# Performance work log

Measured on AMD Instinct MI355X. Metric: run time of the kernel, lower is better.

## Reference

```python
import jax, jax.numpy as jnp
import numpy as np
from jax import lax

silu = jax.nn.silu

def conv2d(x, w, b, pad):
    y = lax.conv_general_dilated(x, w, (1, 1), [(pad, pad), (pad, pad)],
                                 dimension_numbers=('NCHW', 'OIHW', 'NCHW'))
    return y + b[None, :, None, None]

def avgpool2(x):
    B, C, H, W = x.shape
    return x.reshape(B, C, H // 2, 2, W // 2, 2).mean(axis=(3, 5))

def up2x(x):
    # bilinear scale_factor=2, align_corners=True (matches F.interpolate)
    B, C, H, W = x.shape
    Ho, Wo = 2 * H, 2 * W
    ys = jnp.arange(Ho, dtype=x.dtype) * ((H - 1) / (Ho - 1))
    xs = jnp.arange(Wo, dtype=x.dtype) * ((W - 1) / (Wo - 1))
    y0 = jnp.floor(ys).astype(jnp.int32); y1 = jnp.minimum(y0 + 1, H - 1); wy = ys - y0
    x0 = jnp.floor(xs).astype(jnp.int32); x1 = jnp.minimum(x0 + 1, W - 1); wx = xs - x0
    row = x[:, :, y0, :] * (1 - wy)[None, None, :, None] + x[:, :, y1, :] * wy[None, None, :, None]
    return row[:, :, :, x0] * (1 - wx) + row[:, :, :, x1] * wx

def deform_conv2d(x, offset, weight, groups):
    # torchvision DeformConv2d semantics: stride=1, pad=(k-1)//2, dilation=1, no bias
    B, Cin, H, W = x.shape
    Cout, cpg, kh, kw = weight.shape  # cpg = Cin // groups
    K = kh * kw
    OG = offset.shape[1] // (2 * K)   # offset groups
    Cog = Cin // OG
    off = offset.reshape(B, OG, K, 2, H, W)  # (dy, dx) per kernel tap
    ki = jnp.repeat(jnp.arange(kh, dtype=x.dtype) - (kh - 1) // 2, kw)  # [K]
    kj = jnp.tile(jnp.arange(kw, dtype=x.dtype) - (kw - 1) // 2, kh)
    py = off[:, :, :, 0] + jnp.arange(H, dtype=x.dtype)[None, None, None, :, None] + ki[None, None, :, None, None]
    px = off[:, :, :, 1] + jnp.arange(W, dtype=x.dtype)[None, None, None, None, :] + kj[None, None, :, None, None]
    y0f = jnp.floor(py); x0f = jnp.floor(px)
    ly = py - y0f; lx = px - x0f
    y0 = y0f.astype(jnp.int32); x0 = x0f.astype(jnp.int32)
    xg = x.reshape(B, OG, Cog, H * W)

    def corner(yi, xi, wt):
        valid = (yi >= 0) & (yi < H) & (xi >= 0) & (xi < W)
        idx = jnp.clip(yi, 0, H - 1) * W + jnp.clip(xi, 0, W - 1)        # [B,OG,K,H,W]
        idxf = jnp.broadcast_to(idx.reshape(B, OG, 1, K * H * W), (B, OG, Cog, K * H * W))
        v = jnp.take_along_axis(xg, idxf, axis=3).reshape(B, OG, Cog, K, H, W)
        return v * (wt * valid)[:, :, None]

    val = (corner(y0, x0, (1 - ly) * (1 - lx)) + corner(y0, x0 + 1, (1 - ly) * lx)
           + corner(y0 + 1, x0, ly * (1 - lx)) + corner(y0 + 1, x0 + 1, ly * lx))
    # grouped contraction over sampled taps
    valg = val.reshape(B, groups, Cin // groups, K, H, W)
    wg = weight.reshape(groups, Cout // groups, cpg, K)
    return jnp.einsum('bgckhw,gock->bgohw', valg, wg).reshape(B, Cout, H, W)

def setup_inputs() -> dict:
    key = jax.random.key(0)
    ks = iter(jax.random.split(key, 64))
    def w(shape, s=0.05):
        return jax.random.normal(next(ks), shape, jnp.float32) * s
    B, H, W = 4, 512, 512
    d = {'x': jax.random.normal(next(ks), (B, 4, H, W), jnp.float32)}
    # offset estimators (small scale so sampled offsets stay moderate)
    d['eo1_w1'] = w((18, 4, 5, 5), 0.02);  d['eo1_b1'] = w((18,), 0.02)
    d['eo1_w2'] = w((36, 18, 5, 5), 0.02); d['eo1_b2'] = w((36,), 0.02)
    d['dcw1'] = w((2, 2, 3, 3))            # DeformConv2d(4->2, groups=2)
    d['c1d_w1'] = w((4, 2, 3, 3));   d['c1d_b1'] = w((4,))
    d['c1d_w2'] = w((8, 4, 3, 3));   d['c1d_b2'] = w((8,))
    d['eo2_w1'] = w((18, 8, 5, 5), 0.02);  d['eo2_b1'] = w((18,), 0.02)
    d['eo2_w2'] = w((36, 18, 5, 5), 0.02); d['eo2_b2'] = w((36,), 0.02)
    d['dcw2'] = w((8, 4, 3, 3))            # DeformConv2d(8->8, groups=2)
    d['c2d_w1'] = w((12, 8, 3, 3));  d['c2d_b1'] = w((12,))
    d['c2d_w2'] = w((16, 12, 3, 3)); d['c2d_b2'] = w((16,))
    d['eo3_w1'] = w((18, 16, 5, 5), 0.02); d['eo3_b1'] = w((18,), 0.02)
    d['eo3_w2'] = w((36, 18, 5, 5), 0.02); d['eo3_b2'] = w((36,), 0.02)
    d['dcw3'] = w((16, 8, 3, 3))           # DeformConv2d(16->16, groups=2)
    d['c3d_w1'] = w((14, 16, 3, 3)); d['c3d_b1'] = w((14,))
    d['c3d_w2'] = w((12, 14, 3, 3)); d['c3d_b2'] = w((12,))
    d['up2_w'] = w((12, 12, 3, 3));  d['up2_b'] = w((12,))
    d['c2u_w1'] = w((16, 28, 3, 3)); d['c2u_b1'] = w((16,))
    d['c2u_w2'] = w((8, 16, 3, 3));  d['c2u_b2'] = w((8,))
    d['up1_w'] = w((8, 8, 3, 3));    d['up1_b'] = w((8,))
    d['c1u_w1'] = w((8, 16, 3, 3));  d['c1u_b1'] = w((8,))
    d['c1u_w2'] = w((2, 8, 3, 3));   d['c1u_b2'] = w((2,))
    return d

def reference(x, eo1_w1, eo1_b1, eo1_w2, eo1_b2, dcw1, c1d_w1, c1d_b1, c1d_w2, c1d_b2,
              eo2_w1, eo2_b1, eo2_w2, eo2_b2, dcw2, c2d_w1, c2d_b1, c2d_w2, c2d_b2,
              eo3_w1, eo3_b1, eo3_w2, eo3_b2, dcw3, c3d_w1, c3d_b1, c3d_w2, c3d_b2,
              up2_w, up2_b, c2u_w1, c2u_b1, c2u_w2, c2u_b2, up1_w, up1_b,
              c1u_w1, c1u_b1, c1u_w2, c1u_b2):
    def convbasic(h, w1, b1, w2, b2):
        return silu(conv2d(silu(conv2d(h, w1, b1, 1)), w2, b2, 1))
    # level 1 down
    off1 = conv2d(conv2d(x, eo1_w1, eo1_b1, 2), eo1_w2, eo1_b2, 2)
    comp1 = deform_conv2d(x, off1, dcw1, groups=2)
    conv1_d = convbasic(comp1, c1d_w1, c1d_b1, c1d_w2, c1d_b2)
    pool1 = avgpool2(conv1_d)
    # level 2 down
    off2 = conv2d(conv2d(pool1, eo2_w1, eo2_b1, 2), eo2_w2, eo2_b2, 2)
    comp2 = deform_conv2d(pool1, off2, dcw2, groups=2)
    conv2_d = convbasic(comp2, c2d_w1, c2d_b1, c2d_w2, c2d_b2)
    pool2 = avgpool2(conv2_d)
    # level 3 (bottleneck)
    off3 = conv2d(conv2d(pool2, eo3_w1, eo3_b1, 2), eo3_w2, eo3_b2, 2)
    comp3 = deform_conv2d(pool2, off3, dcw3, groups=2)
    conv3_d = convbasic(comp3, c3d_w1, c3d_b1, c3d_w2, c3d_b2)
    # up path
    usmpl2 = silu(conv2d(up2x(conv3_d), up2_w, up2_b, 1))
    conv2_u = convbasic(jnp.concatenate([usmpl2, conv2_d], axis=1), c2u_w1, c2u_b1, c2u_w2, c2u_b2)
    usmpl1 = silu(conv2d(up2x(conv2_u), up1_w, up1_b, 1))
    conv1_u = convbasic(jnp.concatenate([usmpl1, conv1_d], axis=1), c1u_w1, c1u_b1, c1u_w2, c1u_b2)
    return conv1_u
```

## Files before the change

kernel.cpp:

```cpp
#include <hip/hip_runtime.h>
#include <math.h>

#define THREADS 256
typedef __attribute__((ext_vector_type(2))) float f32x2;
typedef __attribute__((ext_vector_type(4))) float f32x4;

__device__ __forceinline__ float silu_f(float v) {
    return v / (1.f + __expf(-v));
}

__device__ __forceinline__ void pk_fma_lo(f32x2& d, f32x2 a, f32x2 b) {
    asm("v_pk_fma_f32 %0, %1, %2, %0 op_sel:[0,0,0] op_sel_hi:[0,1,1]"
        : "+v"(d) : "v"(a), "v"(b));
}
__device__ __forceinline__ void pk_fma_hi(f32x2& d, f32x2 a, f32x2 b) {
    asm("v_pk_fma_f32 %0, %1, %2, %0 op_sel:[1,0,0] op_sel_hi:[1,1,1]"
        : "+v"(d) : "v"(a), "v"(b));
}

struct TEnt { const float* src; int dst; int cin; int cout; int k2; int base; int n; };
struct TTab { TEnt e[40]; int total; };

__global__ __launch_bounds__(THREADS)
void transpose_w_k(TTab t, float* __restrict__ tw) {
    const int i = blockIdx.x * THREADS + threadIdx.x;
    if (i >= t.total) return;
    int j = 0;
    while (i >= t.e[j].base + t.e[j].n) ++j;
    const TEnt e = t.e[j];
    const int local = i - e.base;
    const int co  = local % e.cout;
    const int tmp = local / e.cout;
    const int k   = tmp % e.k2;
    const int ci  = tmp / e.k2;
    tw[e.dst + local] = e.src[(co * e.cin + ci) * e.k2 + k];
}

template<int KS, int PX>
__device__ __forceinline__ void load_row(float* __restrict__ rr,
                                         const float* __restrict__ rp,
                                         bool vy, int x0, int W)
{
    constexpr int PAD = (KS - 1) / 2;
    constexpr int RW = PX + KS - 1;
#pragma unroll
    for (int q = -1; q <= PX / 4; ++q) {
        if (4 * q + 3 + PAD < 0 || 4 * q + PAD >= RW) continue;
        const int xs = x0 + 4 * q;
        float vc[4] = {0.f, 0.f, 0.f, 0.f};
        if (vy && xs >= 0 && xs + 4 <= W) {
            const float4 v = *reinterpret_cast<const float4*>(rp + xs);
            vc[0] = v.x; vc[1] = v.y; vc[2] = v.z; vc[3] = v.w;
        } else if (vy) {
#pragma unroll
            for (int c = 0; c < 4; ++c)
                vc[c] = ((unsigned)(xs + c) < (unsigned)W) ? rp[xs + c] : 0.f;
        }
#pragma unroll
        for (int c = 0; c < 4; ++c) {
            const int t = 4 * q + c + PAD;
            if (t >= 0 && t < RW) rr[t] = vc[c];
        }
    }
}

template<int CIN, int COUT, int KS, int PX, int PHASE, int RW2, int WQ, int NP>
__device__ __forceinline__ void chan_body(
    const float* __restrict__ ip0, const float* __restrict__ sw,
    int cl, int y, int x0, int W, int H, int lw, int total,
    f32x2 (&r2)[2][RW2], f32x4 (&wb)[2][WQ], f32x2 (&acc)[NP][PX])
{
    constexpr int PAD = (KS - 1) / 2;
    constexpr int K2 = KS * KS;
    constexpr int CO_S = (COUT + 3) & ~3;
#pragma unroll
    for (int ky = 0; ky < KS; ++ky) {
        {
            const bool last = (ky + 1 == KS);
            const int ncl = cl + (last ? 1 : 0);
            const int nky = last ? 0 : (ky + 1);
            if (!last || ncl < CIN) {
                const int yy = y + nky - PAD;
                load_row<KS, PX>((float*)r2[(PHASE + ky + 1) & 1],
                                 ip0 + (size_t)ncl * total + (yy << lw),
                                 (unsigned)yy < (unsigned)H, x0, W);
            }
        }
#pragma unroll
        for (int kx = 0; kx < KS; ++kx) {
            const int t = ky * KS + kx;
            const int wc = (PHASE + t) & 1;
            if (t + 1 < K2 || cl + 1 < CIN) {
                const f32x4* __restrict__ nx =
                    (const f32x4*)(sw + (size_t)(cl * K2 + t + 1) * CO_S);
#pragma unroll
                for (int q = 0; q < WQ; ++q) wb[wc ^ 1][q] = nx[q];
            }
#pragma unroll
            for (int q = 0; q < WQ; ++q) {
                const f32x4 w4 = wb[wc][q];
                const f32x2 wlo = __builtin_shufflevector(w4, w4, 0, 1);
                const f32x2 whi = __builtin_shufflevector(w4, w4, 2, 3);
#pragma unroll
                for (int s = 0; s < 2; ++s) {
                    const int p = 2 * q + s;
                    if (p < NP) {
                        const f32x2 wp = s ? whi : wlo;
#pragma unroll
                        for (int j = 0; j < PX; ++j) {
                            const int e = kx + j;
                            if (e & 1) pk_fma_hi(acc[p][j], r2[(PHASE + ky) & 1][e >> 1], wp);
                            else       pk_fma_lo(acc[p][j], r2[(PHASE + ky) & 1][e >> 1], wp);
                        }
                    }
                }
            }
            __builtin_amdgcn_sched_barrier(0);
        }
    }
}

template<int CIN, int COUT, int KS, bool ACT, int PX>
__global__ __launch_bounds__(THREADS)
void conv_sl_k(const float* __restrict__ in, const float* __restrict__ wt,
               const float* __restrict__ bias, float* __restrict__ out,
               int H, int lw, int bs_in, int bs_out, int nb, int nz)
{
    constexpr int PAD = (KS - 1) / 2;
    constexpr int K2 = KS * KS;
    constexpr int CO_S = (COUT + 3) & ~3;
    constexpr int WQ = CO_S / 4;
    constexpr int NP = COUT / 2;
    constexpr int RW = PX + KS - 1;
    constexpr int RW2 = (RW + 1) / 2;
    static_assert(CIN % 2 == 0 && COUT % 2 == 0 && PX % 4 == 0, "");
    __shared__ float sw[CIN * K2 * CO_S];

    int lin = blockIdx.x;
    const int z = lin % nz; lin /= nz;
    const int b = lin % nb; lin /= nb;
    const int xb = lin;

    const float* __restrict__ wz = wt + (size_t)z * (CIN * K2 * COUT);
    const int W = 1 << lw;
    const int total = H << lw;
    const int idx = (xb * THREADS + threadIdx.x) * PX;
    const float* ip0 = in + (size_t)b * bs_in;
    float* op = out + (size_t)b * bs_out + (size_t)z * COUT * total;
    const int x0 = idx & (W - 1);
    const int y  = idx >> lw;

    for (int i = threadIdx.x; i < CIN * K2 * COUT; i += THREADS)
        sw[(i / COUT) * CO_S + i % COUT] = wz[i];
    __syncthreads();

    f32x2 acc[NP][PX];
#pragma unroll
    for (int p = 0; p < NP; ++p) {
        f32x2 bb;
        bb.x = bias[z * COUT + 2 * p];
        bb.y = bias[z * COUT + 2 * p + 1];
#pragma unroll
        for (int j = 0; j < PX; ++j) acc[p][j] = bb;
    }

    f32x2 r2[2][RW2];
    f32x4 wb[2][WQ];
    {
        const int yy = y - PAD;
        load_row<KS, PX>((float*)r2[0], ip0 + (yy << lw),
                         (unsigned)yy < (unsigned)H, x0, W);
        const f32x4* __restrict__ w0 = (const f32x4*)sw;
#pragma unroll
        for (int q = 0; q < WQ; ++q) wb[0][q] = w0[q];
    }

#pragma unroll 1
    for (int c2 = 0; c2 < CIN / 2; ++c2) {
        chan_body<CIN, COUT, KS, PX, 0, RW2, WQ, NP>(ip0, sw, 2 * c2,     y, x0, W, H, lw, total, r2, wb, acc);
        chan_body<CIN, COUT, KS, PX, 1, RW2, WQ, NP>(ip0, sw, 2 * c2 + 1, y, x0, W, H, lw, total, r2, wb, acc);
    }

#pragma unroll
    for (int p = 0; p < NP; ++p) {
#pragma unroll
        for (int h = 0; h < 2; ++h) {
            const int co = 2 * p + h;
#pragma unroll
            for (int j4 = 0; j4 < PX / 4; ++j4) {
                float4 v;
                float a0 = h ? acc[p][4 * j4 + 0].y : acc[p][4 * j4 + 0].x;
                float a1 = h ? acc[p][4 * j4 + 1].y : acc[p][4 * j4 + 1].x;
                float a2 = h ? acc[p][4 * j4 + 2].y : acc[p][4 * j4 + 2].x;
                float a3 = h ? acc[p][4 * j4 + 3].y : acc[p][4 * j4 + 3].x;
                v.x = ACT ? silu_f(a0) : a0;
                v.y = ACT ? silu_f(a1) : a1;
                v.z = ACT ? silu_f(a2) : a2;
                v.w = ACT ? silu_f(a3) : a3;
                *reinterpret_cast<float4*>(op + (size_t)co * total + idx + 4 * j4) = v;
            }
        }
    }
}

template<int CIN, int COUT, int KS, bool ACT, int PX>
__global__ __launch_bounds__(THREADS)
void conv_k(const float* __restrict__ in, const float* __restrict__ wt,
            const float* __restrict__ bias, float* __restrict__ out,
            int H, int lw, int bs_in, int bs_out)
{
    constexpr int PAD = (KS - 1) / 2;
    constexpr int K2 = KS * KS;
    constexpr int CO_S = (COUT + 3) & ~3;
    constexpr int WQ = CO_S / 4;
    constexpr int NP = COUT / 2;
    constexpr int RW = PX + KS - 1;
    constexpr int RW2 = (RW + 1) / 2;
    static_assert(COUT % 2 == 0, "");
    __shared__ float sw[CIN * K2 * CO_S];

    const int W = 1 << lw;
    const int total = H << lw;
    const int idx = (blockIdx.x * THREADS + threadIdx.x) * PX;
    const float* ip0 = in + (size_t)blockIdx.y * bs_in;
    float* op = out + (size_t)blockIdx.y * bs_out;
    const int x0 = idx & (W - 1);
    const int y  = idx >> lw;

    for (int i = threadIdx.x; i < CIN * K2 * COUT; i += THREADS)
        sw[(i / COUT) * CO_S + i % COUT] = wt[i];
    __syncthreads();

    f32x2 acc[NP][PX];
#pragma unroll
    for (int p = 0; p < NP; ++p) {
        f32x2 bb;
        bb.x = bias[2 * p];
        bb.y = bias[2 * p + 1];
#pragma unroll
        for (int j = 0; j < PX; ++j) acc[p][j] = bb;
    }

#pragma unroll 1
    for (int cl = 0; cl < CIN; ++cl) {
        const float* __restrict__ row0 = ip0 + (size_t)cl * total;
        f32x2 r2[KS][RW2];
#pragma unroll
        for (int ky = 0; ky < KS; ++ky) {
            const int yy = y + ky - PAD;
            load_row<KS, PX>((float*)r2[ky], row0 + (yy << lw),
                             (unsigned)yy < (unsigned)H, x0, W);
        }
        const float* __restrict__ wbase = &sw[cl * K2 * CO_S];
#pragma unroll
        for (int t = 0; t < K2; ++t) {
            const int ky = t / KS, kx = t % KS;
            const f32x4* __restrict__ wv = (const f32x4*)(wbase + t * CO_S);
#pragma unroll
            for (int q = 0; q < WQ; ++q) {
                const f32x4 w4 = wv[q];
                const f32x2 wlo = __builtin_shufflevector(w4, w4, 0, 1);
                const f32x2 whi = __builtin_shufflevector(w4, w4, 2, 3);
#pragma unroll
                for (int s = 0; s < 2; ++s) {
                    const int p = 2 * q + s;
                    if (p < NP) {
                        const f32x2 wp = s ? whi : wlo;
#pragma unroll
                        for (int j = 0; j < PX; ++j) {
                            const int e = kx + j;
                            if (e & 1) pk_fma_hi(acc[p][j], r2[ky][e >> 1], wp);
                            else       pk_fma_lo(acc[p][j], r2[ky][e >> 1], wp);
                        }
                    }
                }
            }
            __builtin_amdgcn_sched_barrier(0);
        }
    }

#pragma unroll
    for (int p = 0; p < NP; ++p) {
#pragma unroll
        for (int h = 0; h < 2; ++h) {
            const int co = 2 * p + h;
            if (PX == 2) {
                float2 v;
                float a0 = h ? acc[p][0].y : acc[p][0].x;
                float a1 = h ? acc[p][1].y : acc[p][1].x;
                v.x = ACT ? silu_f(a0) : a0;
                v.y = ACT ? silu_f(a1) : a1;
                *reinterpret_cast<float2*>(op + (size_t)co * total + idx) = v;
            } else {
#pragma unroll
                for (int j4 = 0; j4 < PX / 4; ++j4) {
                    float4 v;
                    float a0 = h ? acc[p][4 * j4 + 0].y : acc[p][4 * j4 + 0].x;
                    float a1 = h ? acc[p][4 * j4 + 1].y : acc[p][4 * j4 + 1].x;
                    float a2 = h ? acc[p][4 * j4 + 2].y : acc[p][4 * j4 + 2].x;
                    float a3 = h ? acc[p][4 * j4 + 3].y : acc[p][4 * j4 + 3].x;
                    v.x = ACT ? silu_f(a0) : a0;
                    v.y = ACT ? silu_f(a1) : a1;
                    v.z = ACT ? silu_f(a2) : a2;
                    v.w = ACT ? silu_f(a3) : a3;
                    *reinterpret_cast<float4*>(op + (size_t)co * total + idx + 4 * j4) = v;
                }
            }
        }
    }
}

template<int CIN, int COUT>
__global__ __launch_bounds__(THREADS)
void dconv_k(const float* __restrict__ in, const float* __restrict__ off,
             const float* __restrict__ twg0, const float* __restrict__ twg1,
             float* __restrict__ out,
             int H, int lw, int bs_in, int bs_off, int bs_out)
{
    constexpr int K = 9;
    constexpr int OG = 2;
    constexpr int COG = CIN / OG;
    constexpr int COUTG = COUT / 2;
    constexpr int NWG = COG * K * COUTG;
    __shared__ float sw[2 * NWG];
    for (int i = threadIdx.x; i < 2 * NWG; i += THREADS)
        sw[i] = (i < NWG) ? twg0[i] : twg1[i - NWG];
    __syncthreads();

    const int W = 1 << lw;
    const int total = H << lw;
    const int idx = blockIdx.x * THREADS + threadIdx.x;
    const float* ip0 = in + (size_t)blockIdx.y * bs_in;
    const float* offp = off + (size_t)blockIdx.y * bs_off;
    float* op = out + (size_t)blockIdx.y * bs_out;
    const int x = idx & (W - 1);
    const int y = idx >> lw;

    float acc[COUT];
#pragma unroll
    for (int co = 0; co < COUT; ++co) acc[co] = 0.f;

#pragma unroll
    for (int og = 0; og < OG; ++og) {
#pragma unroll
        for (int k = 0; k < K; ++k) {
            const int ki = k / 3 - 1;
            const int kj = k % 3 - 1;
            const float dy = offp[(size_t)(((og * K + k) * 2 + 0)) * total + idx];
            const float dx = offp[(size_t)(((og * K + k) * 2 + 1)) * total + idx];
            const float py = dy + (float)(y + ki);
            const float px = dx + (float)(x + kj);
            const float y0f = floorf(py), x0f = floorf(px);
            const float ly = py - y0f, lx = px - x0f;
            const int y0 = (int)y0f, x0 = (int)x0f;
            const int y1 = y0 + 1, x1 = x0 + 1;
            const bool vy0 = (unsigned)y0 < (unsigned)H;
            const bool vy1 = (unsigned)y1 < (unsigned)H;
            const bool vx0 = (unsigned)x0 < (unsigned)W;
            const bool vx1 = (unsigned)x1 < (unsigned)W;
            const int cy0 = min(max(y0, 0), H - 1), cy1 = min(max(y1, 0), H - 1);
            const int cx0 = min(max(x0, 0), W - 1), cx1 = min(max(x1, 0), W - 1);
            const int i00 = (cy0 << lw) + cx0, i01 = (cy0 << lw) + cx1;
            const int i10 = (cy1 << lw) + cx0, i11 = (cy1 << lw) + cx1;
            const float f00 = (vy0 && vx0) ? (1.f - ly) * (1.f - lx) : 0.f;
            const float f01 = (vy0 && vx1) ? (1.f - ly) * lx : 0.f;
            const float f10 = (vy1 && vx0) ? ly * (1.f - lx) : 0.f;
            const float f11 = (vy1 && vx1) ? ly * lx : 0.f;
            const float* swg = &sw[og * NWG];
#pragma unroll
            for (int c = 0; c < COG; ++c) {
                const float* __restrict__ ip = ip0 + (size_t)(og * COG + c) * total;
                const float v = f00 * ip[i00] + f01 * ip[i01]
                              + f10 * ip[i10] + f11 * ip[i11];
                const float* __restrict__ wr = &swg[(c * K + k) * COUTG];
#pragma unroll
                for (int col = 0; col < COUTG; ++col)
                    acc[og * COUTG + col] = fmaf(v, wr[col], acc[og * COUTG + col]);
            }
        }
    }

#pragma unroll
    for (int co = 0; co < COUT; ++co)
        op[(size_t)co * total + idx] = acc[co];
}

__global__ __launch_bounds__(THREADS)
void avgpool_k(const float* __restrict__ in, float* __restrict__ out,
               int n, int lt, int lwo, int bsi, int bso)
{
    const int idx = blockIdx.x * THREADS + threadIdx.x;
    if (idx >= n) return;
    const float* ip0 = in + (size_t)blockIdx.y * bsi;
    float* op = out + (size_t)blockIdx.y * bso;
    const int c = idx >> lt;
    const int r = idx & ((1 << lt) - 1);
    const int oy = r >> lwo;
    const int ox = r & ((1 << lwo) - 1);
    const int Wi = 2 << lwo;
    const float* ip = ip0 + ((size_t)c << (lt + 2)) + ((size_t)(2 * oy) << (lwo + 1)) + 2 * ox;
    const float2 t = *reinterpret_cast<const float2*>(ip);
    const float2 b = *reinterpret_cast<const float2*>(ip + Wi);
    op[idx] = 0.25f * (t.x + t.y + b.x + b.y);
}

__global__ __launch_bounds__(THREADS)
void up2x_k(const float* __restrict__ in, float* __restrict__ out,
            int n, int lt, int lwo, int Hin, int bsi, int bso)
{
    const int idx = blockIdx.x * THREADS + threadIdx.x;
    if (idx >= n) return;
    const float* ip0 = in + (size_t)blockIdx.y * bsi;
    float* op = out + (size_t)blockIdx.y * bso;
    const int c = idx >> lt;
    const int r = idx & ((1 << lt) - 1);
    const int oy = r >> lwo;
    const int ox = r & ((1 << lwo) - 1);
    const int W = 1 << (lwo - 1);
    const int H = Hin;
    const float s = (float)(H - 1) / (float)(2 * H - 1);
    const float fy = (float)oy * s;
    const float fx = (float)ox * s;
    const int y0 = (int)fy;
    const int x0 = (int)fx;
    const int y1 = min(y0 + 1, H - 1);
    const int x1 = min(x0 + 1, W - 1);
    const float wy = fy - (float)y0;
    const float wx = fx - (float)x0;
    const float* ip = ip0 + ((size_t)c << (lt - 2));
    const float v00 = ip[y0 * W + x0], v01 = ip[y0 * W + x1];
    const float v10 = ip[y1 * W + x0], v11 = ip[y1 * W + x1];
    op[idx] = (v00 * (1.f - wy) + v10 * wy) * (1.f - wx)
            + (v01 * (1.f - wy) + v11 * wy) * wx;
}

__global__ __launch_bounds__(THREADS)
void copy_k(float4* __restrict__ dst, const float4* __restrict__ src,
            int n4, int bsd, int bss)
{
    const int i = blockIdx.x * THREADS + threadIdx.x;
    if (i >= n4) return;
    dst[(size_t)blockIdx.y * bsd + i] = src[(size_t)blockIdx.y * bss + i];
}


extern "C" void kernel_launch(void* const* d_in, const int* in_sizes, int n_in,
                              void* d_out, int out_size, void* d_ws, size_t ws_size,
                              hipStream_t stream) {
    const float* x      = (const float*)d_in[0];
    const float* eo1_b1 = (const float*)d_in[2];
    const float* eo1_b2 = (const float*)d_in[4];
    const float* c1d_b1 = (const float*)d_in[7];
    const float* c1d_b2 = (const float*)d_in[9];
    const float* eo2_b1 = (const float*)d_in[11];
    const float* eo2_b2 = (const float*)d_in[13];
    const float* c2d_b1 = (const float*)d_in[16];
    const float* c2d_b2 = (const float*)d_in[18];
    const float* eo3_b1 = (const float*)d_in[20];
    const float* eo3_b2 = (const float*)d_in[22];
    const float* c3d_b1 = (const float*)d_in[25];
    const float* c3d_b2 = (const float*)d_in[27];
    const float* up2_b  = (const float*)d_in[29];
    const float* c2u_b1 = (const float*)d_in[31];
    const float* c2u_b2 = (const float*)d_in[33];
    const float* up1_b  = (const float*)d_in[35];
    const float* c1u_b1 = (const float*)d_in[37];
    const float* c1u_b2 = (const float*)d_in[39];

    float* out = (float*)d_out;
    float* wsf = (float*)d_ws;

    constexpr int H1 = 512, A1 = H1 * H1;
    constexpr int H2 = 256, A2 = H2 * H2;
    constexpr int H3 = 128, A3 = H3 * H3;
    constexpr int TW_FLOATS = 81920;
    constexpr int SLOT = 58 * A1;

    const int widx[34]  = {1, 1, 1,  3, 3, 3, 3, 3,  6, 8,
                           10, 10, 10,  12, 12, 12, 12, 12,  15, 17,
                           19,  21, 21, 21, 21, 21,  24, 26,
                           28, 30, 32, 34, 36, 38};
    const int wcin[34]  = {4, 4, 4,  18, 18, 18, 18, 18,  2, 4,
                           8, 8, 8,  18, 18, 18, 18, 18,  8, 12,
                           16,  18, 18, 18, 18, 18,  16, 14,
                           12, 28, 16, 8, 16, 8};
    const int wcout[34] = {6, 6, 6,  8, 8, 8, 8, 4,  4, 8,
                           6, 6, 6,  8, 8, 8, 8, 4,  12, 16,
                           18,  8, 8, 8, 8, 4,  14, 12,
                           12, 16, 8, 8, 8, 2};
    const int wk2[34]   = {25, 25, 25,  25, 25, 25, 25, 25,  9, 9,
                           25, 25, 25,  25, 25, 25, 25, 25,  9, 9,
                           25,  25, 25, 25, 25, 25,  9, 9,
                           9, 9, 9, 9, 9, 9};
    const int wsoff[34] = {0, 600, 1200,  0, 3600, 7200, 10800, 14400,  0, 0,
                           0, 1200, 2400,  0, 3600, 7200, 10800, 14400,  0, 0,
                           0,  0, 3600, 7200, 10800, 14400,  0, 0,
                           0, 0, 0, 0, 0, 0};
    const int cont[34]  = {1, 1, 0,  1, 1, 1, 0, 0,  0, 0,
                           1, 1, 0,  1, 1, 1, 0, 0,  0, 0,
                           0,  1, 1, 1, 0, 0,  0, 0,
                           0, 0, 0, 0, 0, 0};
    TTab tab;
    const float* tw[40];
    int off = 0, base = 0;
    for (int i = 0; i < 34; ++i) {
        const int n = wcin[i] * wcout[i] * wk2[i];
        tab.e[i].src = (const float*)d_in[widx[i]] + wsoff[i];
        tab.e[i].dst = off; tab.e[i].cin = wcin[i]; tab.e[i].cout = wcout[i];
        tab.e[i].k2 = wk2[i]; tab.e[i].base = base; tab.e[i].n = n;
        tw[i] = wsf + off;
        off = cont[i] ? (off + n) : ((off + n + 63) & ~63);
        base += n;
    }
    const int didx[3]   = {5, 14, 23};
    const int dcoutg[3] = {1, 4, 8};
    const int dcpg[3]   = {2, 4, 8};
    for (int i = 0; i < 3; ++i) {
        for (int g = 0; g < 2; ++g) {
            const int e = 34 + 2 * i + g;
            const int n = dcoutg[i] * dcpg[i] * 9;
            tab.e[e].src = (const float*)d_in[didx[i]] + (size_t)g * n;
            tab.e[e].dst = off; tab.e[e].cin = dcpg[i]; tab.e[e].cout = dcoutg[i];
            tab.e[e].k2 = 9; tab.e[e].base = base; tab.e[e].n = n;
            tw[e] = wsf + off;
            off = (off + n + 63) & ~63;
            base += n;
        }
    }
    tab.total = base;
    transpose_w_k<<<(base + THREADS - 1) / THREADS, THREADS, 0, stream>>>(tab, wsf);

    int B = 4;
    while (B > 1 && ws_size < ((size_t)TW_FLOATS + (size_t)B * SLOT) * sizeof(float)) B >>= 1;

    auto run_all = [&](int Bc, float* slot, int SB,
                       const float* xin, int xbs, float* outp, int obs) {
        float* S0 = slot;
        float* S1 = S0 + 36 * A1;
        float* S2 = S1 + 18 * A1;
        float* P  = S2 + 2 * A1;
        float* L1 = S1 + 10 * A1;
        float* L2 = S0 + 32 * A1;
        auto gs = [&](int n, int px, int z) { return dim3((n / (px * THREADS)) * Bc * z); };
        auto gp = [&](int n, int px) { return dim3(n / (px * THREADS), Bc); };
        auto g1 = [&](int n) { return dim3((n + THREADS - 1) / THREADS, Bc); };

        conv_sl_k<4, 6, 5, false, 8><<<gs(A1, 8, 3), THREADS, 0, stream>>>(xin, tw[0], eo1_b1, S1, H1, 9, xbs, SB, Bc, 3);
        conv_sl_k<18, 8, 5, false, 8><<<gs(A1, 8, 4), THREADS, 0, stream>>>(S1, tw[3], eo1_b2, S0, H1, 9, SB, SB, Bc, 4);
        conv_sl_k<18, 4, 5, false, 8><<<gs(A1, 8, 1), THREADS, 0, stream>>>(S1, tw[7], eo1_b2 + 32, S0 + 32 * A1, H1, 9, SB, SB, Bc, 1);
        dconv_k<4, 2><<<g1(A1), THREADS, 0, stream>>>(xin, S0, tw[34], tw[35], S2, H1, 9, xbs, SB, SB);
        conv_k<2, 4, 3, true, 4><<<gp(A1, 4), THREADS, 0, stream>>>(S2, tw[8], c1d_b1, S1, H1, 9, SB, SB);
        conv_k<4, 8, 3, true, 4><<<gp(A1, 4), THREADS, 0, stream>>>(S1, tw[9], c1d_b2, L1, H1, 9, SB, SB);
        avgpool_k<<<g1(8 * A2), THREADS, 0, stream>>>(L1, P, 8 * A2, 16, 8, SB, SB);

        conv_sl_k<8, 6, 5, false, 8><<<gs(A2, 8, 3), THREADS, 0, stream>>>(P, tw[10], eo2_b1, S1, H2, 8, SB, SB, Bc, 3);
        conv_sl_k<18, 8, 5, false, 8><<<gs(A2, 8, 4), THREADS, 0, stream>>>(S1, tw[13], eo2_b2, S0, H2, 8, SB, SB, Bc, 4);
        conv_sl_k<18, 4, 5, false, 8><<<gs(A2, 8, 1), THREADS, 0, stream>>>(S1, tw[17], eo2_b2 + 32, S0 + 32 * A2, H2, 8, SB, SB, Bc, 1);
        dconv_k<8, 8><<<g1(A2), THREADS, 0, stream>>>(P, S0, tw[36], tw[37], S2, H2, 8, SB, SB, SB);
        conv_k<8, 12, 3, true, 2><<<gp(A2, 2), THREADS, 0, stream>>>(S2, tw[18], c2d_b1, S1, H2, 8, SB, SB);
        conv_k<12, 16, 3, true, 2><<<gp(A2, 2), THREADS, 0, stream>>>(S1, tw[19], c2d_b2, L2, H2, 8, SB, SB);
        avgpool_k<<<g1(16 * A3), THREADS, 0, stream>>>(L2, P, 16 * A3, 14, 7, SB, SB);

        conv_k<16, 18, 5, false, 2><<<gp(A3, 2), THREADS, 0, stream>>>(P, tw[20], eo3_b1, S1, H3, 7, SB, SB);
        conv_sl_k<18, 8, 5, false, 4><<<gs(A3, 4, 4), THREADS, 0, stream>>>(S1, tw[21], eo3_b2, S0, H3, 7, SB, SB, Bc, 4);
        conv_sl_k<18, 4, 5, false, 4><<<gs(A3, 4, 1), THREADS, 0, stream>>>(S1, tw[25], eo3_b2 + 32, S0 + 32 * A3, H3, 7, SB, SB, Bc, 1);
        dconv_k<16, 16><<<g1(A3), THREADS, 0, stream>>>(P, S0, tw[38], tw[39], S2, H3, 7, SB, SB, SB);
        conv_k<16, 14, 3, true, 2><<<gp(A3, 2), THREADS, 0, stream>>>(S2, tw[26], c3d_b1, S1, H3, 7, SB, SB);
        conv_k<14, 12, 3, true, 2><<<gp(A3, 2), THREADS, 0, stream>>>(S1, tw[27], c3d_b2, S2, H3, 7, SB, SB);

        up2x_k<<<g1(12 * A2), THREADS, 0, stream>>>(S2, S0, 12 * A2, 16, 8, H3, SB, SB);
        conv_k<12, 12, 3, true, 2><<<gp(A2, 2), THREADS, 0, stream>>>(S0, tw[28], up2_b, S1, H2, 8, SB, SB);
        copy_k<<<g1(4 * A2), THREADS, 0, stream>>>((float4*)(S1 + 12 * A2), (const float4*)L2,
                                                   4 * A2, SB / 4, SB / 4);
        conv_k<28, 16, 3, true, 2><<<gp(A2, 2), THREADS, 0, stream>>>(S1, tw[29], c2u_b1, S0, H2, 8, SB, SB);
        conv_k<16, 8, 3, true, 2><<<gp(A2, 2), THREADS, 0, stream>>>(S0, tw[30], c2u_b2, S2, H2, 8, SB, SB);

        up2x_k<<<g1(8 * A1), THREADS, 0, stream>>>(S2, S0, 8 * A1, 18, 9, H2, SB, SB);
        conv_k<8, 8, 3, true, 4><<<gp(A1, 4), THREADS, 0, stream>>>(S0, tw[31], up1_b, S0 + 8 * A1, H1, 9, SB, SB);
        copy_k<<<g1(2 * A1), THREADS, 0, stream>>>((float4*)(S0 + 16 * A1), (const float4*)L1,
                                                   2 * A1, SB / 4, SB / 4);
        conv_k<16, 8, 3, true, 4><<<gp(A1, 4), THREADS, 0, stream>>>(S0 + 8 * A1, tw[32], c1u_b1, S1, H1, 9, SB, SB);
        conv_k<8, 2, 3, true, 4><<<gp(A1, 4), THREADS, 0, stream>>>(S1, tw[33], c1u_b2, outp, H1, 9, SB, obs);
    };

    for (int g = 0; g < 4; g += B)
        run_all(B, wsf + TW_FLOATS, SLOT,
                x + (size_t)g * 4 * A1, 4 * A1,
                out + (size_t)g * 2 * A1, 2 * A1);
}
```

Baseline: 1.529 ms.

## Split offset convs into uniform 4-channel slices and double pixels per thread

The second offset conv at levels 1 and 2 was split into four 8-channel slices plus one 4-channel slice. It is now nine uniform 4-channel slices launched as a single kernel with 16 pixels per thread, which drops the extra remainder launch. The weight transpose table grows from 34 to 42 conv entries to match. Most 3x3 convs also double their pixels-per-thread tile (2→4, 4→8) to reuse loaded rows across more outputs. The cost is higher register pressure and fewer blocks, which may lower occupancy.

Result: no change. 1.525 ms (-0.2%).

```diff
diff --git a/kernel.cpp b/kernel.cpp
--- a/kernel.cpp
+++ b/kernel.cpp
@@ -19,7 +19,7 @@
 }
 
 struct TEnt { const float* src; int dst; int cin; int cout; int k2; int base; int n; };
-struct TTab { TEnt e[40]; int total; };
+struct TTab { TEnt e[48]; int total; };
 
 __global__ __launch_bounds__(THREADS)
 void transpose_w_k(TTab t, float* __restrict__ tw) {
@@ -475,35 +475,66 @@
     constexpr int H3 = 128, A3 = H3 * H3;
     constexpr int TW_FLOATS = 81920;
     constexpr int SLOT = 58 * A1;
-
-    const int widx[34]  = {1, 1, 1,  3, 3, 3, 3, 3,  6, 8,
-                           10, 10, 10,  12, 12, 12, 12, 12,  15, 17,
-                           19,  21, 21, 21, 21, 21,  24, 26,
-                           28, 30, 32, 34, 36, 38};
-    const int wcin[34]  = {4, 4, 4,  18, 18, 18, 18, 18,  2, 4,
-                           8, 8, 8,  18, 18, 18, 18, 18,  8, 12,
-                           16,  18, 18, 18, 18, 18,  16, 14,
-                           12, 28, 16, 8, 16, 8};
-    const int wcout[34] = {6, 6, 6,  8, 8, 8, 8, 4,  4, 8,
-                           6, 6, 6,  8, 8, 8, 8, 4,  12, 16,
-                           18,  8, 8, 8, 8, 4,  14, 12,
-                           12, 16, 8, 8, 8, 2};
-    const int wk2[34]   = {25, 25, 25,  25, 25, 25, 25, 25,  9, 9,
-                           25, 25, 25,  25, 25, 25, 25, 25,  9, 9,
-                           25,  25, 25, 25, 25, 25,  9, 9,
-                           9, 9, 9, 9, 9, 9};
-    const int wsoff[34] = {0, 600, 1200,  0, 3600, 7200, 10800, 14400,  0, 0,
-                           0, 1200, 2400,  0, 3600, 7200, 10800, 14400,  0, 0,
-                           0,  0, 3600, 7200, 10800, 14400,  0, 0,
-                           0, 0, 0, 0, 0, 0};
-    const int cont[34]  = {1, 1, 0,  1, 1, 1, 0, 0,  0, 0,
-                           1, 1, 0,  1, 1, 1, 0, 0,  0, 0,
-                           0,  1, 1, 1, 0, 0,  0, 0,
-                           0, 0, 0, 0, 0, 0};
+    constexpr int NCONV = 42;
+
+    const int widx[NCONV]  = {1, 1, 1,
+                              3, 3, 3, 3, 3, 3, 3, 3, 3,
+                              6, 8,
+                              10, 10, 10,
+                              12, 12, 12, 12, 12, 12, 12, 12, 12,
+                              15, 17,
+                              19,
+                              21, 21, 21, 21, 21,
+                              24, 26, 28, 30, 32, 34, 36, 38};
+    const int wcin[NCONV]  = {4, 4, 4,
+                              18, 18, 18, 18, 18, 18, 18, 18, 18,
+                              2, 4,
+                              8, 8, 8,
+                              18, 18, 18, 18, 18, 18, 18, 18, 18,
+                              8, 12,
+                              16,
+                              18, 18, 18, 18, 18,
+                              16, 14, 12, 28, 16, 8, 16, 8};
+    const int wcout[NCONV] = {6, 6, 6,
+                              4, 4, 4, 4, 4, 4, 4, 4, 4,
+                              4, 8,
+                              6, 6, 6,
+                              4, 4, 4, 4, 4, 4, 4, 4, 4,
+                              12, 16,
+                              18,
+                              8, 8, 8, 8, 4,
+                              14, 12, 12, 16, 8, 8, 8, 2};
+    const int wk2[NCONV]   = {25, 25, 25,
+                              25, 25, 25, 25, 25, 25, 25, 25, 25,
+                              9, 9,
+                              25, 25, 25,
+                              25, 25, 25, 25, 25, 25, 25, 25, 25,
+                              9, 9,
+                              25,
+                              25, 25, 25, 25, 25,
+                              9, 9, 9, 9, 9, 9, 9, 9};
+    const int wsoff[NCONV] = {0, 600, 1200,
+                              0, 1800, 3600, 5400, 7200, 9000, 10800, 12600, 14400,
+                              0, 0,
+                              0, 1200, 2400,
+                              0, 1800, 3600, 5400, 7200, 9000, 10800, 12600, 14400,
+                              0, 0,
+                              0,
+                              0, 3600, 7200, 10800, 14400,
+                              0, 0, 0, 0, 0, 0, 0, 0};
+    const int cont[NCONV]  = {1, 1, 0,
+                              1, 1, 1, 1, 1, 1, 1, 1, 0,
+                              0, 0,
+                              1, 1, 0,
+                              1, 1, 1, 1, 1, 1, 1, 1, 0,
+                              0, 0,
+                              0,
+                              1, 1, 1, 0, 0,
+                              0, 0, 0, 0, 0, 0, 0, 0};
     TTab tab;
-    const float* tw[40];
+    const float* tw[48];
     int off = 0, base = 0;
-    for (int i = 0; i < 34; ++i) {
+    for (int i = 0; i < NCONV; ++i) {
         const int n = wcin[i] * wcout[i] * wk2[i];
         tab.e[i].src = (const float*)d_in[widx[i]] + wsoff[i];
         tab.e[i].dst = off; tab.e[i].cin = wcin[i]; tab.e[i].cout = wcout[i];
@@ -517,7 +548,7 @@
     const int dcpg[3]   = {2, 4, 8};
     for (int i = 0; i < 3; ++i) {
         for (int g = 0; g < 2; ++g) {
-            const int e = 34 + 2 * i + g;
+            const int e = NCONV + 2 * i + g;
             const int n = dcoutg[i] * dcpg[i] * 9;
             tab.e[e].src = (const float*)d_in[didx[i]] + (size_t)g * n;
             tab.e[e].dst = off; tab.e[e].cin = dcpg[i]; tab.e[e].cout = dcoutg[i];
@@ -546,41 +577,39 @@
         auto g1 = [&](int n) { return dim3((n + THREADS - 1) / THREADS, Bc); };
 
         conv_sl_k<4, 6, 5, false, 8><<<gs(A1, 8, 3), THREADS, 0, stream>>>(xin, tw[0], eo1_b1, S1, H1, 9, xbs, SB, Bc, 3);
-        conv_sl_k<18, 8, 5, false, 8><<<gs(A1, 8, 4), THREADS, 0, stream>>>(S1, tw[3], eo1_b2, S0, H1, 9, SB, SB, Bc, 4);
-        conv_sl_k<18, 4, 5, false, 8><<<gs(A1, 8, 1), THREADS, 0, stream>>>(S1, tw[7], eo1_b2 + 32, S0 + 32 * A1, H1, 9, SB, SB, Bc, 1);
-        dconv_k<4, 2><<<g1(A1), THREADS, 0, stream>>>(xin, S0, tw[34], tw[35], S2, H1, 9, xbs, SB, SB);
-        conv_k<2, 4, 3, true, 4><<<gp(A1, 4), THREADS, 0, stream>>>(S2, tw[8], c1d_b1, S1, H1, 9, SB, SB);
-        conv_k<4, 8, 3, true, 4><<<gp(A1, 4), THREADS, 0, stream>>>(S1, tw[9], c1d_b2, L1, H1, 9, SB, SB);
+        conv_sl_k<18, 4, 5, false, 16><<<gs(A1, 16, 9), THREADS, 0, stream>>>(S1, tw[3], eo1_b2, S0, H1, 9, SB, SB, Bc, 9);
+        dconv_k<4, 2><<<g1(A1), THREADS, 0, stream>>>(xin, S0, tw[NCONV + 0], tw[NCONV + 1], S2, H1, 9, xbs, SB, SB);
+        conv_k<2, 4, 3, true, 8><<<gp(A1, 8), THREADS, 0, stream>>>(S2, tw[12], c1d_b1, S1, H1, 9, SB, SB);
+        conv_k<4, 8, 3, true, 8><<<gp(A1, 8), THREADS, 0, stream>>>(S1, tw[13], c1d_b2, L1, H1, 9, SB, SB);
         avgpool_k<<<g1(8 * A2), THREADS, 0, stream>>>(L1, P, 8 * A2, 16, 8, SB, SB);
 
-        conv_sl_k<8, 6, 5, false, 8><<<gs(A2, 8, 3), THREADS, 0, stream>>>(P, tw[10], eo2_b1, S1, H2, 8, SB, SB, Bc, 3);
-        conv_sl_k<18, 8, 5, false, 8><<<gs(A2, 8, 4), THREADS, 0, stream>>>(S1, tw[13], eo2_b2, S0, H2, 8, SB, SB, Bc, 4);
-        conv_sl_k<18, 4, 5, false, 8><<<gs(A2, 8, 1), THREADS, 0, stream>>>(S1, tw[17], eo2_b2 + 32, S0 + 32 * A2, H2, 8, SB, SB, Bc, 1);
-        dconv_k<8, 8><<<g1(A2), THREADS, 0, stream>>>(P, S0, tw[36], tw[37], S2, H2, 8, SB, SB, SB);
-        conv_k<8, 12, 3, true, 2><<<gp(A2, 2), THREADS, 0, stream>>>(S2, tw[18], c2d_b1, S1, H2, 8, SB, SB);
-        conv_k<12, 16, 3, true, 2><<<gp(A2, 2), THREADS, 0, stream>>>(S1, tw[19], c2d_b2, L2, H2, 8, SB, SB);
+        conv_sl_k<8, 6, 5, false, 8><<<gs(A2, 8, 3), THREADS, 0, stream>>>(P, tw[14], eo2_b1, S1, H2, 8, SB, SB, Bc, 3);
+        conv_sl_k<18, 4, 5, false, 16><<<gs(A2, 16, 9), THREADS, 0, stream>>>(S1, tw[17], eo2_b2, S0, H2, 8, SB, SB, Bc, 9);
+        dconv_k<8, 8><<<g1(A2), THREADS, 0, stream>>>(P, S0, tw[NCONV + 2], tw[NCONV + 3], S2, H2, 8, SB, SB, SB);
+        conv_k<8, 12, 3, true, 4><<<gp(A2, 4), THREADS, 0, stream>>>(S2, tw[26], c2d_b1, S1, H2, 8, SB, SB);
+        conv_k<12, 16, 3, true, 4><<<gp(A2, 4), THREADS, 0, stream>>>(S1, tw[27], c2d_b2, L2, H2, 8, SB, SB);
         avgpool_k<<<g1(16 * A3), THREADS, 0, stream>>>(L2, P, 16 * A3, 14, 7, SB, SB);
 
-        conv_k<16, 18, 5, false, 2><<<gp(A3, 2), THREADS, 0, stream>>>(P, tw[20], eo3_b1, S1, H3, 7, SB, SB);
-        conv_sl_k<18, 8, 5, false, 4><<<gs(A3, 4, 4), THREADS, 0, stream>>>(S1, tw[21], eo3_b2, S0, H3, 7, SB, SB, Bc, 4);
-        conv_sl_k<18, 4, 5, false, 4><<<gs(A3, 4, 1), THREADS, 0, stream>>>(S1, tw[25], eo3_b2 + 32, S0 + 32 * A3, H3, 7, SB, SB, Bc, 1);
-        dconv_k<16, 16><<<g1(A3), THREADS, 0, stream>>>(P, S0, tw[38], tw[39], S2, H3, 7, SB, SB, SB);
-        conv_k<16, 14, 3, true, 2><<<gp(A3, 2), THREADS, 0, stream>>>(S2, tw[26], c3d_b1, S1, H3, 7, SB, SB);
-        conv_k<14, 12, 3, true, 2><<<gp(A3, 2), THREADS, 0, stream>>>(S1, tw[27], c3d_b2, S2, H3, 7, SB, SB);
+        conv_k<16, 18, 5, false, 2><<<gp(A3, 2), THREADS, 0, stream>>>(P, tw[28], eo3_b1, S1, H3, 7, SB, SB);
+        conv_sl_k<18, 8, 5, false, 4><<<gs(A3, 4, 4), THREADS, 0, stream>>>(S1, tw[29], eo3_b2, S0, H3, 7, SB, SB, Bc, 4);
+        conv_sl_k<18, 4, 5, false, 4><<<gs(A3, 4, 1), THREADS, 0, stream>>>(S1, tw[33], eo3_b2 + 32, S0 + 32 * A3, H3, 7, SB, SB, Bc, 1);
+        dconv_k<16, 16><<<g1(A3), THREADS, 0, stream>>>(P, S0, tw[NCONV + 4], tw[NCONV + 5], S2, H3, 7, SB, SB, SB);
+        conv_k<16, 14, 3, true, 2><<<gp(A3, 2), THREADS, 0, stream>>>(S2, tw[34], c3d_b1, S1, H3, 7, SB, SB);
+        conv_k<14, 12, 3, true, 2><<<gp(A3, 2), THREADS, 0, stream>>>(S1, tw[35], c3d_b2, S2, H3, 7, SB, SB);
 
         up2x_k<<<g1(12 * A2), THREADS, 0, stream>>>(S2, S0, 12 * A2, 16, 8, H3, SB, SB);
-        conv_k<12, 12, 3, true, 2><<<gp(A2, 2), THREADS, 0, stream>>>(S0, tw[28], up2_b, S1, H2, 8, SB, SB);
+        conv_k<12, 12, 3, true, 4><<<gp(A2, 4), THREADS, 0, stream>>>(S0, tw[36], up2_b, S1, H2, 8, SB, SB);
         copy_k<<<g1(4 * A2), THREADS, 0, stream>>>((float4*)(S1 + 12 * A2), (const float4*)L2,
                                                    4 * A2, SB / 4, SB / 4);
-        conv_k<28, 16, 3, true, 2><<<gp(A2, 2), THREADS, 0, stream>>>(S1, tw[29], c2u_b1, S0, H2, 8, SB, SB);
-        conv_k<16, 8, 3, true, 2><<<gp(A2, 2), THREADS, 0, stream>>>(S0, tw[30], c2u_b2, S2, H2, 8, SB, SB);
+        conv_k<28, 16, 3, true, 4><<<gp(A2, 4), THREADS, 0, stream>>>(S1, tw[37], c2u_b1, S0, H2, 8, SB, SB);
+        conv_k<16, 8, 3, true, 4><<<gp(A2, 4), THREADS, 0, stream>>>(S0, tw[38], c2u_b2, S2, H2, 8, SB, SB);
 
         up2x_k<<<g1(8 * A1), THREADS, 0, stream>>>(S2, S0, 8 * A1, 18, 9, H2, SB, SB);
-        conv_k<8, 8, 3, true, 4><<<gp(A1, 4), THREADS, 0, stream>>>(S0, tw[31], up1_b, S0 + 8 * A1, H1, 9, SB, SB);
+        conv_k<8, 8, 3, true, 8><<<gp(A1, 8), THREADS, 0, stream>>>(S0, tw[39], up1_b, S0 + 8 * A1, H1, 9, SB, SB);
         copy_k<<<g1(2 * A1), THREADS, 0, stream>>>((float4*)(S0 + 16 * A1), (const float4*)L1,
                                                    2 * A1, SB / 4, SB / 4);
-        conv_k<16, 8, 3, true, 4><<<gp(A1, 4), THREADS, 0, stream>>>(S0 + 8 * A1, tw[32], c1u_b1, S1, H1, 9, SB, SB);
-        conv_k<8, 2, 3, true, 4><<<gp(A1, 4), THREADS, 0, stream>>>(S1, tw[33], c1u_b2, outp, H1, 9, SB, obs);
+        conv_k<16, 8, 3, true, 8><<<gp(A1, 8), THREADS, 0, stream>>>(S0 + 8 * A1, tw[40], c1u_b1, S1, H1, 9, SB, SB);
+        conv_k<8, 2, 3, true, 8><<<gp(A1, 8), THREADS, 0, stream>>>(S1, tw[41], c1u_b2, outp, H1, 9, SB, obs);
     };
 
     for (int g = 0; g < 4; g += B)
```
